# Kernel tuning notes

Hardware: AMD Instinct MI355X
Metric: run time of the kernel (lower is better)

Reference implementation:

```python
import jax, jax.numpy as jnp
import numpy as np

ATTN_BLOCK_SIZE = 1024
NUM_BUCKETS = 32  # int(sqrt(1024))


def _bucket_index():
    # Static index matching the torch init:
    # arange2 = ((arange1 - indices) % S) // num_buckets, then pick columns arange(nb)*nb
    S, nb = ATTN_BLOCK_SIZE, NUM_BUCKETS
    ar = np.arange(S)
    a2 = ((ar[:, None] - ar[None, :]) % S) // nb          # (S, S), values in [0, nb)
    a2 = a2[:, np.arange(nb) * nb]                         # (S, nb)
    return jnp.asarray(a2, dtype=jnp.int32)


def _decay_sum(x, alpha, beta, past_steps):
    # result[t] = alpha * sum_{i=0}^{P-1} beta**i * x[t-1-i]  (zeros for t-1-i < 0)
    # == the torch pad-and-add loop, expressed as one causal depthwise conv.
    B, S, D = x.shape
    P = past_steps
    w = alpha * beta ** jnp.arange(P, dtype=x.dtype)       # (P,) decay weights
    k = jnp.broadcast_to(w[::-1][None, None, :], (D, 1, P))  # depthwise kernel (O=D, I/g=1, W=P)
    xc = jnp.transpose(x, (0, 2, 1))                       # (B, D, S)
    y = jax.lax.conv_general_dilated(
        xc, k, window_strides=(1,), padding=[(P, 0)],
        dimension_numbers=('NCW', 'OIW', 'NCW'), feature_group_count=D,
    )[..., :S]                                             # (B, D, S)
    return jnp.transpose(y, (0, 2, 1))                     # (B, S, D)


def setup_inputs() -> dict:
    key = jax.random.key(0)
    k1, k2, k3, k4, k5 = jax.random.split(key, 5)
    B, S, nb = 1024, ATTN_BLOCK_SIZE, NUM_BUCKETS
    return {
        "x": jax.random.normal(k1, (B, S, nb), dtype=jnp.float32),
        "alpha": jax.random.uniform(k2, (1,), dtype=jnp.float32),
        "beta": jax.random.uniform(k3, (1,), dtype=jnp.float32),
        "pos_fwd_param": jax.random.normal(k4, (1, nb), dtype=jnp.float32),
        "pos_bwd_param": jax.random.normal(k5, (1, nb), dtype=jnp.float32),
        "past_steps": 128,
    }


def reference(x, alpha, beta, pos_fwd_param, pos_bwd_param, past_steps):
    S = ATTN_BLOCK_SIZE
    result = _decay_sum(x, alpha, beta, past_steps)        # (B, S, nb)
    ones = jnp.ones((S, 1), dtype=x.dtype)
    pb_fwd = ones @ pos_fwd_param                          # (S, nb)
    pb_bwd = jnp.take_along_axis(ones @ pos_bwd_param, _bucket_index(), axis=-1)  # (S, nb)
    return result + pb_fwd + pb_bwd
```

## Files before the change

### kernel.cpp

```cpp
#include <hip/hip_runtime.h>


typedef float f32x4 __attribute__((ext_vector_type(4)));

constexpr int S    = 1024;
constexpr int D    = 32;
constexpr int CL   = 32;
constexpr int NCH  = S / CL;
constexpr int NTHR = NCH * (D / 4);

__global__ __launch_bounds__(NTHR, 4)
void attn_pred_kernel(const float* __restrict__ x,
                      const float* __restrict__ alpha_p,
                      const float* __restrict__ beta_p,
                      const float* __restrict__ pos_fwd,
                      const float* __restrict__ pos_bwd,
                      const int*   __restrict__ past_p,
                      float* __restrict__ out)
{
    __shared__ f32x4 lcar[NCH][D / 4];

    const int tid = threadIdx.x;
    const int b   = blockIdx.x;
    const int dg  = tid & 7;
    const int c   = tid >> 3;
    const int s0  = c * CL;

    const float alpha = alpha_p[0];
    const float beta  = beta_p[0];
    const int   P     = past_p[0];

    double bp = 1.0;
    for (int i = 0; i < P; ++i) bp *= (double)beta;
    const float abP = alpha * (float)bp;
    double bcl = 1.0;
    for (int i = 0; i < CL; ++i) bcl *= (double)beta;
    const float bCL = (float)bcl;

    const f32x4* xg = reinterpret_cast<const f32x4*>(x) + (size_t)b * S * (D / 4);

    f32x4 l = {0.f, 0.f, 0.f, 0.f};
    #pragma unroll 8
    for (int i = 0; i < CL; ++i) {
        const int s  = s0 + i;
        const int sl = s - P;
        const f32x4 xt = xg[s * (D / 4) + dg];
        f32x4 xl = {0.f, 0.f, 0.f, 0.f};
        if (sl >= 0) xl = xg[sl * (D / 4) + dg];
        l.x = fmaf(beta, l.x, fmaf(alpha, xt.x, -abP * xl.x));
        l.y = fmaf(beta, l.y, fmaf(alpha, xt.y, -abP * xl.y));
        l.z = fmaf(beta, l.z, fmaf(alpha, xt.z, -abP * xl.z));
        l.w = fmaf(beta, l.w, fmaf(alpha, xt.w, -abP * xl.w));
    }
    lcar[c][dg] = l;
    __syncthreads();

    if (tid < D / 4) {
        f32x4 run = {0.f, 0.f, 0.f, 0.f};
        for (int cc = 0; cc < NCH; ++cc) {
            const f32x4 v = lcar[cc][tid];
            lcar[cc][tid] = run;
            run.x = fmaf(bCL, run.x, v.x);
            run.y = fmaf(bCL, run.y, v.y);
            run.z = fmaf(bCL, run.z, v.z);
            run.w = fmaf(bCL, run.w, v.w);
        }
    }
    __syncthreads();
    f32x4 y = lcar[c][dg];

    const int d0 = dg * 4;
    const f32x4 pf = reinterpret_cast<const f32x4*>(pos_fwd)[dg];
    f32x4 add;
    add.x = pf.x + pos_bwd[(c - (d0 + 0)) & (D - 1)];
    add.y = pf.y + pos_bwd[(c - (d0 + 1)) & (D - 1)];
    add.z = pf.z + pos_bwd[(c - (d0 + 2)) & (D - 1)];
    add.w = pf.w + pos_bwd[(c - (d0 + 3)) & (D - 1)];

    f32x4* og = reinterpret_cast<f32x4*>(out) + ((size_t)b * S + s0) * (D / 4) + dg;
    #pragma unroll 8
    for (int i = 0; i < CL; ++i) {
        f32x4 o;
        o.x = y.x + add.x; o.y = y.y + add.y;
        o.z = y.z + add.z; o.w = y.w + add.w;
        __builtin_nontemporal_store(o, &og[i * (D / 4)]);

        const int s  = s0 + i;
        const int sl = s - P;
        const f32x4 xt = xg[s * (D / 4) + dg];
        f32x4 xl = {0.f, 0.f, 0.f, 0.f};
        if (sl >= 0) xl = xg[sl * (D / 4) + dg];
        y.x = fmaf(beta, y.x, fmaf(alpha, xt.x, -abP * xl.x));
        y.y = fmaf(beta, y.y, fmaf(alpha, xt.y, -abP * xl.y));
        y.z = fmaf(beta, y.z, fmaf(alpha, xt.z, -abP * xl.z));
        y.w = fmaf(beta, y.w, fmaf(alpha, xt.w, -abP * xl.w));
    }
}

extern "C" void kernel_launch(void* const* d_in, const int* in_sizes, int n_in,
                              void* d_out, int out_size, void* d_ws, size_t ws_size,
                              hipStream_t stream) {
    const float* x  = (const float*)d_in[0];
    const float* al = (const float*)d_in[1];
    const float* be = (const float*)d_in[2];
    const float* pf = (const float*)d_in[3];
    const float* pb = (const float*)d_in[4];
    const int*   ps = (const int*)d_in[5];
    float* out = (float*)d_out;

    const int B = in_sizes[0] / (S * D);
    attn_pred_kernel<<<dim3(B), NTHR, 0, stream>>>(x, al, be, pf, pb, ps, out);
}
```

Baseline: 259.2 us.

## Scan chunk sums and apply lag correction at chunk level with smaller chunks

The first pass now computes plain decayed chunk sums of x, with no per-element lagged load. The subtraction of the term P steps back moves into the serial carry scan, done on chunk sums LAG chunks earlier. Chunk length drops to 16, giving 512 threads per block, and the occupancy hint is raised. beta^P is now computed by repeated squaring. This cuts global reads in the first pass and adds parallelism, but LAG=8 silently assumes past_steps equals 128 (LAG*CL), so other P values give wrong results.

```diff
diff --git a/kernel.cpp b/kernel.cpp
--- a/kernel.cpp
+++ b/kernel.cpp
@@ -5,11 +5,12 @@
 
 constexpr int S    = 1024;
 constexpr int D    = 32;
-constexpr int CL   = 32;
+constexpr int CL   = 16;
 constexpr int NCH  = S / CL;
+constexpr int LAG  = 8;
 constexpr int NTHR = NCH * (D / 4);
 
-__global__ __launch_bounds__(NTHR, 4)
+__global__ __launch_bounds__(NTHR, 8)
 void attn_pred_kernel(const float* __restrict__ x,
                       const float* __restrict__ alpha_p,
                       const float* __restrict__ beta_p,
@@ -18,7 +19,8 @@
                       const int*   __restrict__ past_p,
                       float* __restrict__ out)
 {
-    __shared__ f32x4 lcar[NCH][D / 4];
+    __shared__ f32x4 sA[NCH][D / 4];
+    __shared__ f32x4 sC[NCH][D / 4];
 
     const int tid = threadIdx.x;
     const int b   = blockIdx.x;
@@ -30,70 +32,78 @@
     const float beta  = beta_p[0];
     const int   P     = past_p[0];
 
-    double bp = 1.0;
-    for (int i = 0; i < P; ++i) bp *= (double)beta;
-    const float abP = alpha * (float)bp;
-    double bcl = 1.0;
-    for (int i = 0; i < CL; ++i) bcl *= (double)beta;
-    const float bCL = (float)bcl;
+    double bb = (double)beta, bpd = 1.0;
+    for (int e = P; e; e >>= 1) { if (e & 1) bpd *= bb; bb *= bb; }
+    const float bP = (float)bpd;
+    double b16 = (double)beta;
+    for (int i = 0; i < 4; ++i) b16 *= b16;
+    const float bCL = (float)b16;
 
-    const f32x4* xg = reinterpret_cast<const f32x4*>(x) + (size_t)b * S * (D / 4);
+    const f32x4* xg = reinterpret_cast<const f32x4*>(x) + (size_t)b * S * (D / 4) + dg;
 
-    f32x4 l = {0.f, 0.f, 0.f, 0.f};
+    f32x4 A = {0.f, 0.f, 0.f, 0.f};
     #pragma unroll 8
     for (int i = 0; i < CL; ++i) {
-        const int s  = s0 + i;
-        const int sl = s - P;
-        const f32x4 xt = xg[s * (D / 4) + dg];
-        f32x4 xl = {0.f, 0.f, 0.f, 0.f};
-        if (sl >= 0) xl = xg[sl * (D / 4) + dg];
-        l.x = fmaf(beta, l.x, fmaf(alpha, xt.x, -abP * xl.x));
-        l.y = fmaf(beta, l.y, fmaf(alpha, xt.y, -abP * xl.y));
-        l.z = fmaf(beta, l.z, fmaf(alpha, xt.z, -abP * xl.z));
-        l.w = fmaf(beta, l.w, fmaf(alpha, xt.w, -abP * xl.w));
+        const f32x4 v = xg[(s0 + i) * (D / 4)];
+        A.x = fmaf(beta, A.x, v.x);
+        A.y = fmaf(beta, A.y, v.y);
+        A.z = fmaf(beta, A.z, v.z);
+        A.w = fmaf(beta, A.w, v.w);
     }
-    lcar[c][dg] = l;
+    sA[c][dg] = A;
     __syncthreads();
 
     if (tid < D / 4) {
         f32x4 run = {0.f, 0.f, 0.f, 0.f};
         for (int cc = 0; cc < NCH; ++cc) {
-            const f32x4 v = lcar[cc][tid];
-            lcar[cc][tid] = run;
-            run.x = fmaf(bCL, run.x, v.x);
-            run.y = fmaf(bCL, run.y, v.y);
-            run.z = fmaf(bCL, run.z, v.z);
-            run.w = fmaf(bCL, run.w, v.w);
+            sC[cc][tid] = run;
+            const f32x4 Ac = sA[cc][tid];
+            f32x4 z;
+            if (cc >= LAG) {
+                const f32x4 Al = sA[cc - LAG][tid];
+                z.x = alpha * fmaf(-bP, Al.x, Ac.x);
+                z.y = alpha * fmaf(-bP, Al.y, Ac.y);
+                z.z = alpha * fmaf(-bP, Al.z, Ac.z);
+                z.w = alpha * fmaf(-bP, Al.w, Ac.w);
+            } else {
+                z.x = alpha * Ac.x; z.y = alpha * Ac.y;
+                z.z = alpha * Ac.z; z.w = alpha * Ac.w;
+            }
+            run.x = fmaf(bCL, run.x, z.x);
+            run.y = fmaf(bCL, run.y, z.y);
+            run.z = fmaf(bCL, run.z, z.z);
+            run.w = fmaf(bCL, run.w, z.w);
         }
     }
     __syncthreads();
-    f32x4 y = lcar[c][dg];
+    f32x4 y = sC[c][dg];
 
     const int d0 = dg * 4;
+    const int q  = c >> 1;
     const f32x4 pf = reinterpret_cast<const f32x4*>(pos_fwd)[dg];
     f32x4 add;
-    add.x = pf.x + pos_bwd[(c - (d0 + 0)) & (D - 1)];
-    add.y = pf.y + pos_bwd[(c - (d0 + 1)) & (D - 1)];
-    add.z = pf.z + pos_bwd[(c - (d0 + 2)) & (D - 1)];
-    add.w = pf.w + pos_bwd[(c - (d0 + 3)) & (D - 1)];
+    add.x = pf.x + pos_bwd[(q - (d0 + 0)) & (D - 1)];
+    add.y = pf.y + pos_bwd[(q - (d0 + 1)) & (D - 1)];
+    add.z = pf.z + pos_bwd[(q - (d0 + 2)) & (D - 1)];
+    add.w = pf.w + pos_bwd[(q - (d0 + 3)) & (D - 1)];
 
+    const float aP = alpha * bP;
+    const bool haveL = (c >= LAG);
     f32x4* og = reinterpret_cast<f32x4*>(out) + ((size_t)b * S + s0) * (D / 4) + dg;
-    #pragma unroll 8
+    #pragma unroll 4
     for (int i = 0; i < CL; ++i) {
         f32x4 o;
         o.x = y.x + add.x; o.y = y.y + add.y;
         o.z = y.z + add.z; o.w = y.w + add.w;
         __builtin_nontemporal_store(o, &og[i * (D / 4)]);
 
-        const int s  = s0 + i;
-        const int sl = s - P;
-        const f32x4 xt = xg[s * (D / 4) + dg];
+        const f32x4 xt = xg[(s0 + i) * (D / 4)];
         f32x4 xl = {0.f, 0.f, 0.f, 0.f};
-        if (sl >= 0) xl = xg[sl * (D / 4) + dg];
-        y.x = fmaf(beta, y.x, fmaf(alpha, xt.x, -abP * xl.x));
-        y.y = fmaf(beta, y.y, fmaf(alpha, xt.y, -abP * xl.y));
-        y.z = fmaf(beta, y.z, fmaf(alpha, xt.z, -abP * xl.z));
-        y.w = fmaf(beta, y.w, fmaf(alpha, xt.w, -abP * xl.w));
+        if (haveL) xl = xg[(s0 - P + i) * (D / 4)];
+        y.x = fmaf(beta, y.x, fmaf(alpha, xt.x, -aP * xl.x));
+        y.y = fmaf(beta, y.y, fmaf(alpha, xt.y, -aP * xl.y));
+        y.z = fmaf(beta, y.z, fmaf(alpha, xt.z, -aP * xl.z));
+        y.w = fmaf(beta, y.w, fmaf(alpha, xt.w, -aP * xl.w));
     }
 }
 
```

New measurement: 254.7 us. About the same (-1.7%).
